# Kernel optimization log

Measured on AMD Instinct MI355X. Metric: run time of the kernel, lower is better.

Reference implementation:

```python
import jax, jax.numpy as jnp
import numpy as np


def setup_inputs() -> dict:
    key = jax.random.key(0)
    k1, k2, k3 = jax.random.split(key, 3)
    B, Cin, Cout, L, K = 16, 64, 64, 65536, 3
    return {
        "x": jax.random.normal(k1, (B, Cin, L), dtype=jnp.float32),
        "alpha": jnp.zeros((1, Cin, 1), dtype=jnp.float32),
        "weight": jax.random.normal(k2, (Cout, Cin, K), dtype=jnp.float32),
        "weight_scale": jnp.ones((Cout, 1, 1), dtype=jnp.float32),
        "bias": jax.random.normal(k3, (Cout,), dtype=jnp.float32),
        "beta": jnp.ones((1, Cout, 1), dtype=jnp.float32),
        "gamma": jnp.zeros((1, Cout, 1), dtype=jnp.float32),
        "zeta": jnp.zeros((1, Cout, 1), dtype=jnp.float32),
    }


def _rsign(x, alpha):
    # forward: sign(x - alpha) in {-1,+1}; backward: identity w.r.t. x (STE)
    signed = jnp.where(x >= alpha, 1.0, -1.0).astype(x.dtype)
    return x + jax.lax.stop_gradient(signed - x)


def _clipped_ste_sign(w):
    # forward: sign(w); backward: grad passes only where |w| <= 1 (Bi-RealNet)
    w_bin = jnp.sign(w)
    mask = (jnp.abs(w) <= 1.0).astype(w.dtype)
    wm = w * mask
    return jax.lax.stop_gradient(w_bin) + wm - jax.lax.stop_gradient(wm)


def _rprelu(x, beta, gamma, zeta):
    xs = x - gamma
    return jnp.where(x > gamma, xs + zeta, beta * xs + zeta)


def reference(x, alpha, weight, weight_scale, bias, beta, gamma, zeta):
    # RSign -> scaled binary conv1d (stride=1, pad=1) -> RPReLU
    xb = _rsign(x, alpha)                        # [B,Cin,L], values +-1
    wb = _clipped_ste_sign(weight) * weight_scale  # [Cout,Cin,K]
    y = jax.lax.conv_general_dilated(
        xb, wb, window_strides=(1,), padding=[(1, 1)],
        dimension_numbers=("NCH", "OIH", "NCH"))  # [B,Cout,L]
    y = y + bias[None, :, None]
    return _rprelu(y, beta, gamma, zeta)
```

## Files before the change

### kernel.cpp

```cpp
#include <hip/hip_runtime.h>

#define LLEN 65536
#define CIN 64
#define COUT 64
#define LTILE 1024

typedef float f32x4 __attribute__((ext_vector_type(4)));
typedef unsigned long long u64;

struct __align__(64) WRec {
    u64 p0, p1, p2;
    float A;
    float S;
    float Bv, G, Z;
    float f0, f2;
    float pad[3];
};

__global__ void pack_weights(const float* __restrict__ w,
                             const float* __restrict__ wscale,
                             const float* __restrict__ bias,
                             const float* __restrict__ beta,
                             const float* __restrict__ gamma,
                             const float* __restrict__ zeta,
                             WRec* __restrict__ rec) {
    int co = threadIdx.x;
    if (co >= COUT) return;
    u64 p[3];
    int nnz[3], ntot = 0;
    for (int k = 0; k < 3; ++k) {
        u64 pos = 0ull, nz = 0ull;
        for (int ci = 0; ci < CIN; ++ci) {
            float wv = w[co * (CIN * 3) + ci * 3 + k];
            pos |= ((u64)(wv > 0.0f)) << ci;
            nz  |= ((u64)(wv != 0.0f)) << ci;
        }
        p[k] = pos;
        nnz[k] = __popcll(nz);
        ntot += nnz[k];
    }
    WRec r;
    float s = wscale[co];
    r.p0 = p[0]; r.p1 = p[1]; r.p2 = p[2];
    r.A  = s * (float)ntot + bias[co];
    r.S  = -2.0f * s;
    r.Bv = beta[co]; r.G = gamma[co]; r.Z = zeta[co];
    r.f0 = 0.5f * (float)nnz[0];
    r.f2 = 0.5f * (float)nnz[2];
    r.pad[0] = r.pad[1] = r.pad[2] = 0.0f;
    rec[co] = r;
}

__device__ __forceinline__ float rprelu(float y, float B, float G, float Z) {
    float xs = y - G;
    return (y > G) ? (xs + Z) : fmaf(B, xs, Z);
}

template <int EDGE>
__device__ __forceinline__ void co_loop(const WRec* __restrict__ rec,
                                        u64 xq0, u64 xq1, u64 xq2,
                                        u64 xq3, u64 xq4, u64 xq5,
                                        bool fixlane, float* __restrict__ outp) {
    #pragma unroll 4
    for (int co = 0; co < COUT; ++co) {
        const WRec r = rec[co];
        float fx = (float)(__popcll(xq0 ^ r.p0) + __popcll(xq1 ^ r.p1)
                         + __popcll(xq2 ^ r.p2));
        float fy = (float)(__popcll(xq1 ^ r.p0) + __popcll(xq2 ^ r.p1)
                         + __popcll(xq3 ^ r.p2));
        float fz = (float)(__popcll(xq2 ^ r.p0) + __popcll(xq3 ^ r.p1)
                         + __popcll(xq4 ^ r.p2));
        float fw = (float)(__popcll(xq3 ^ r.p0) + __popcll(xq4 ^ r.p1)
                         + __popcll(xq5 ^ r.p2));
        if (EDGE == 1 && fixlane)
            fx = (float)(__popcll(xq1 ^ r.p1) + __popcll(xq2 ^ r.p2)) + r.f0;
        if (EDGE == 2 && fixlane)
            fw = (float)(__popcll(xq3 ^ r.p0) + __popcll(xq4 ^ r.p1)) + r.f2;
        f32x4 o;
        o.x = rprelu(fmaf(r.S, fx, r.A), r.Bv, r.G, r.Z);
        o.y = rprelu(fmaf(r.S, fy, r.A), r.Bv, r.G, r.Z);
        o.z = rprelu(fmaf(r.S, fz, r.A), r.Bv, r.G, r.Z);
        o.w = rprelu(fmaf(r.S, fw, r.A), r.Bv, r.G, r.Z);
        __builtin_nontemporal_store(o, (f32x4*)(outp + (size_t)co * LLEN));
    }
}

__global__ void __launch_bounds__(256, 2) bconv_kernel(
        const float* __restrict__ x,
        const float* __restrict__ alpha,
        const WRec* __restrict__ rec,
        float* __restrict__ out) {
    __shared__ u64 xw[LTILE + 2];

    const int t = threadIdx.x;
    const int b = blockIdx.y;
    const int lbase = blockIdx.x * LTILE;
    const float* xrow = x + (size_t)b * CIN * LLEN;

    const float* xb = xrow + lbase + 4 * t;
    u64 w0 = 0, w1 = 0, w2 = 0, w3 = 0;
    #pragma unroll
    for (int batch = 0; batch < 4; ++batch) {
        f32x4 buf[16];
        #pragma unroll
        for (int j = 0; j < 16; ++j)
            buf[j] = *(const f32x4*)(xb + (size_t)(batch * 16 + j) * LLEN);
        #pragma unroll
        for (int j = 0; j < 16; ++j) {
            const int ci = batch * 16 + j;
            const float a = alpha[ci];
            w0 |= ((u64)(buf[j].x >= a)) << ci;
            w1 |= ((u64)(buf[j].y >= a)) << ci;
            w2 |= ((u64)(buf[j].z >= a)) << ci;
            w3 |= ((u64)(buf[j].w >= a)) << ci;
        }
    }
    xw[4 * t + 1] = w0;
    xw[4 * t + 2] = w1;
    xw[4 * t + 3] = w2;
    xw[4 * t + 4] = w3;

    if (t < 64) {
        int l = lbase - 1;
        float v = (l >= 0) ? xrow[(size_t)t * LLEN + l] : 0.0f;
        u64 word = __ballot(v >= alpha[t]);
        if (t == 0) xw[0] = word;
    } else if (t < 128) {
        int ci = t - 64;
        int l = lbase + LTILE;
        float v = (l < LLEN) ? xrow[(size_t)ci * LLEN + l] : 0.0f;
        u64 word = __ballot(v >= alpha[ci]);
        if (ci == 0) xw[LTILE + 1] = word;
    }
    __syncthreads();

    const u64 xq0 = xw[4 * t + 0], xq1 = xw[4 * t + 1],
              xq2 = xw[4 * t + 2], xq3 = xw[4 * t + 3],
              xq4 = xw[4 * t + 4], xq5 = xw[4 * t + 5];
    float* outp = out + (size_t)b * COUT * LLEN + lbase + 4 * t;

    if (blockIdx.x == 0)
        co_loop<1>(rec, xq0, xq1, xq2, xq3, xq4, xq5, t == 0, outp);
    else if (blockIdx.x == gridDim.x - 1)
        co_loop<2>(rec, xq0, xq1, xq2, xq3, xq4, xq5, t == 255, outp);
    else
        co_loop<0>(rec, xq0, xq1, xq2, xq3, xq4, xq5, false, outp);
}

extern "C" void kernel_launch(void* const* d_in, const int* in_sizes, int n_in,
                              void* d_out, int out_size, void* d_ws, size_t ws_size,
                              hipStream_t stream) {
    const float* x      = (const float*)d_in[0];
    const float* alpha  = (const float*)d_in[1];
    const float* w      = (const float*)d_in[2];
    const float* wscale = (const float*)d_in[3];
    const float* bias   = (const float*)d_in[4];
    const float* beta   = (const float*)d_in[5];
    const float* gamma  = (const float*)d_in[6];
    const float* zeta   = (const float*)d_in[7];
    float* out = (float*)d_out;

    WRec* rec = (WRec*)d_ws;

    pack_weights<<<1, 64, 0, stream>>>(w, wscale, bias, beta, gamma, zeta, rec);

    dim3 grid(LLEN / LTILE, 16);
    bconv_kernel<<<grid, 256, 0, stream>>>(x, alpha, rec, out);
}
```

Baseline: 109.2 us.

## Process two L-tiles per block, overlapping next tile's input loads with current outputs

Each block now handles two consecutive 1024-wide tiles. The x loads for the second tile are issued in chunks interleaved with the output computation and stores of the first tile, so reads and writes overlap within a block. The halo word between the two tiles is reused from shared memory instead of being reloaded. The cost is half as many blocks, which lowers parallelism and tail balance, plus more register pressure from holding the load buffers during the popcount loop.

```diff
diff --git a/kernel.cpp b/kernel.cpp
--- a/kernel.cpp
+++ b/kernel.cpp
@@ -4,6 +4,7 @@
 #define CIN 64
 #define COUT 64
 #define LTILE 1024
+#define TPB 2
 
 typedef float f32x4 __attribute__((ext_vector_type(4)));
 typedef unsigned long long u64;
@@ -57,12 +58,13 @@
 }
 
 template <int EDGE>
-__device__ __forceinline__ void co_loop(const WRec* __restrict__ rec,
-                                        u64 xq0, u64 xq1, u64 xq2,
-                                        u64 xq3, u64 xq4, u64 xq5,
-                                        bool fixlane, float* __restrict__ outp) {
+__device__ __forceinline__ void co_range(const WRec* __restrict__ rec,
+                                         int co0, int co1,
+                                         u64 xq0, u64 xq1, u64 xq2,
+                                         u64 xq3, u64 xq4, u64 xq5,
+                                         bool fixlane, float* __restrict__ outp) {
     #pragma unroll 4
-    for (int co = 0; co < COUT; ++co) {
+    for (int co = co0; co < co1; ++co) {
         const WRec r = rec[co];
         float fx = (float)(__popcll(xq0 ^ r.p0) + __popcll(xq1 ^ r.p1)
                          + __popcll(xq2 ^ r.p2));
@@ -85,66 +87,113 @@
     }
 }
 
+template <int EDGE0>
+__device__ __forceinline__ void iter0(const WRec* __restrict__ rec,
+                                      const float* __restrict__ xb1,
+                                      const float* __restrict__ alpha,
+                                      u64 a0, u64 a1, u64 a2, u64 a3, u64 a4, u64 a5,
+                                      bool fix0, float* __restrict__ outp0,
+                                      u64& n0, u64& n1, u64& n2, u64& n3) {
+    #pragma unroll
+    for (int q = 0; q < 4; ++q) {
+        f32x4 buf[16];
+        #pragma unroll
+        for (int jj = 0; jj < 16; ++jj)
+            buf[jj] = *(const f32x4*)(xb1 + (size_t)(q * 16 + jj) * LLEN);
+        co_range<EDGE0>(rec, q * 16, q * 16 + 16, a0, a1, a2, a3, a4, a5,
+                        fix0, outp0);
+        #pragma unroll
+        for (int jj = 0; jj < 16; ++jj) {
+            const int ci = q * 16 + jj;
+            const float a = alpha[ci];
+            n0 |= ((u64)(buf[jj].x >= a)) << ci;
+            n1 |= ((u64)(buf[jj].y >= a)) << ci;
+            n2 |= ((u64)(buf[jj].z >= a)) << ci;
+            n3 |= ((u64)(buf[jj].w >= a)) << ci;
+        }
+    }
+}
+
 __global__ void __launch_bounds__(256, 2) bconv_kernel(
         const float* __restrict__ x,
         const float* __restrict__ alpha,
         const WRec* __restrict__ rec,
         float* __restrict__ out) {
-    __shared__ u64 xw[LTILE + 2];
+    __shared__ u64 xw[2][LTILE + 2];
 
     const int t = threadIdx.x;
     const int b = blockIdx.y;
-    const int lbase = blockIdx.x * LTILE;
+    const int lbase0 = blockIdx.x * (LTILE * TPB);
+    const int lbase1 = lbase0 + LTILE;
     const float* xrow = x + (size_t)b * CIN * LLEN;
 
-    const float* xb = xrow + lbase + 4 * t;
-    u64 w0 = 0, w1 = 0, w2 = 0, w3 = 0;
-    #pragma unroll
-    for (int batch = 0; batch < 4; ++batch) {
-        f32x4 buf[16];
-        #pragma unroll
-        for (int j = 0; j < 16; ++j)
-            buf[j] = *(const f32x4*)(xb + (size_t)(batch * 16 + j) * LLEN);
-        #pragma unroll
-        for (int j = 0; j < 16; ++j) {
-            const int ci = batch * 16 + j;
+    {
+        const float* xb = xrow + lbase0 + 4 * t;
+        u64 w0 = 0, w1 = 0, w2 = 0, w3 = 0;
+        #pragma unroll 16
+        for (int ci = 0; ci < CIN; ++ci) {
+            const f32x4 v = *(const f32x4*)(xb + (size_t)ci * LLEN);
             const float a = alpha[ci];
-            w0 |= ((u64)(buf[j].x >= a)) << ci;
-            w1 |= ((u64)(buf[j].y >= a)) << ci;
-            w2 |= ((u64)(buf[j].z >= a)) << ci;
-            w3 |= ((u64)(buf[j].w >= a)) << ci;
-        }
-    }
-    xw[4 * t + 1] = w0;
-    xw[4 * t + 2] = w1;
-    xw[4 * t + 3] = w2;
-    xw[4 * t + 4] = w3;
-
-    if (t < 64) {
-        int l = lbase - 1;
-        float v = (l >= 0) ? xrow[(size_t)t * LLEN + l] : 0.0f;
-        u64 word = __ballot(v >= alpha[t]);
-        if (t == 0) xw[0] = word;
-    } else if (t < 128) {
+            w0 |= ((u64)(v.x >= a)) << ci;
+            w1 |= ((u64)(v.y >= a)) << ci;
+            w2 |= ((u64)(v.z >= a)) << ci;
+            w3 |= ((u64)(v.w >= a)) << ci;
+        }
+        xw[0][4 * t + 1] = w0;
+        xw[0][4 * t + 2] = w1;
+        xw[0][4 * t + 3] = w2;
+        xw[0][4 * t + 4] = w3;
+
+        if (t < 64) {
+            int l = lbase0 - 1;
+            float v = (l >= 0) ? xrow[(size_t)t * LLEN + l] : 0.0f;
+            u64 word = __ballot(v >= alpha[t]);
+            if (t == 0) xw[0][0] = word;
+        } else if (t < 128) {
+            int ci = t - 64;
+            float v = xrow[(size_t)ci * LLEN + (lbase0 + LTILE)];
+            u64 word = __ballot(v >= alpha[ci]);
+            if (ci == 0) xw[0][LTILE + 1] = word;
+        }
+    }
+    __syncthreads();
+
+    const u64 a0 = xw[0][4 * t + 0], a1 = xw[0][4 * t + 1],
+              a2 = xw[0][4 * t + 2], a3 = xw[0][4 * t + 3],
+              a4 = xw[0][4 * t + 4], a5 = xw[0][4 * t + 5];
+    float* outp0 = out + (size_t)b * COUT * LLEN + lbase0 + 4 * t;
+    float* outp1 = outp0 + LTILE;
+
+    const float* xb1 = xrow + lbase1 + 4 * t;
+    u64 n0 = 0, n1 = 0, n2 = 0, n3 = 0;
+    if (blockIdx.x == 0)
+        iter0<1>(rec, xb1, alpha, a0, a1, a2, a3, a4, a5, t == 0, outp0,
+                 n0, n1, n2, n3);
+    else
+        iter0<0>(rec, xb1, alpha, a0, a1, a2, a3, a4, a5, false, outp0,
+                 n0, n1, n2, n3);
+
+    xw[1][4 * t + 1] = n0;
+    xw[1][4 * t + 2] = n1;
+    xw[1][4 * t + 3] = n2;
+    xw[1][4 * t + 4] = n3;
+    if (t == 0) xw[1][0] = xw[0][LTILE];
+    if (t >= 64 && t < 128) {
         int ci = t - 64;
-        int l = lbase + LTILE;
+        int l = lbase1 + LTILE;
         float v = (l < LLEN) ? xrow[(size_t)ci * LLEN + l] : 0.0f;
         u64 word = __ballot(v >= alpha[ci]);
-        if (ci == 0) xw[LTILE + 1] = word;
+        if (ci == 0) xw[1][LTILE + 1] = word;
     }
     __syncthreads();
 
-    const u64 xq0 = xw[4 * t + 0], xq1 = xw[4 * t + 1],
-              xq2 = xw[4 * t + 2], xq3 = xw[4 * t + 3],
-              xq4 = xw[4 * t + 4], xq5 = xw[4 * t + 5];
-    float* outp = out + (size_t)b * COUT * LLEN + lbase + 4 * t;
-
-    if (blockIdx.x == 0)
-        co_loop<1>(rec, xq0, xq1, xq2, xq3, xq4, xq5, t == 0, outp);
-    else if (blockIdx.x == gridDim.x - 1)
-        co_loop<2>(rec, xq0, xq1, xq2, xq3, xq4, xq5, t == 255, outp);
+    const u64 c0 = xw[1][4 * t + 0], c1 = xw[1][4 * t + 1],
+              c2 = xw[1][4 * t + 2], c3 = xw[1][4 * t + 3],
+              c4 = xw[1][4 * t + 4], c5 = xw[1][4 * t + 5];
+    if (blockIdx.x == gridDim.x - 1)
+        co_range<2>(rec, 0, COUT, c0, c1, c2, c3, c4, c5, t == 255, outp1);
     else
-        co_loop<0>(rec, xq0, xq1, xq2, xq3, xq4, xq5, false, outp);
+        co_range<0>(rec, 0, COUT, c0, c1, c2, c3, c4, c5, false, outp1);
 }
 
 extern "C" void kernel_launch(void* const* d_in, const int* in_sizes, int n_in,
@@ -164,6 +213,6 @@
 
     pack_weights<<<1, 64, 0, stream>>>(w, wscale, bias, beta, gamma, zeta, rec);
 
-    dim3 grid(LLEN / LTILE, 16);
+    dim3 grid(LLEN / (LTILE * TPB), 16);
     bconv_kernel<<<grid, 256, 0, stream>>>(x, alpha, rec, out);
 }
```

Result: slower. 139.4 us (+27.7%).
